# Optimization experiments

Measured on AMD Instinct MI355X. Metric: run time of the kernel, lower is better.

## Reference

```python
import jax, jax.numpy as jnp
import numpy as np

N_NODES = 200000
N_GRAPHS = 512

def gcn_conv(x, src, dst, W, b):
    # PyG GCNConv: add self-loops, symmetric normalization, linear, scatter-add
    n = x.shape[0]
    loop = jnp.arange(n)
    s = jnp.concatenate([src, loop])
    d = jnp.concatenate([dst, loop])
    deg = jax.ops.segment_sum(jnp.ones_like(d, dtype=x.dtype), d, num_segments=n)
    dinv = jnp.where(deg > 0, jax.lax.rsqrt(deg), 0.0)
    norm = dinv[s] * dinv[d]                      # [E+n]
    h = x @ W                                     # [n, out]
    msg = h[s] * norm[:, None]                    # gather on source nodes
    return jax.ops.segment_sum(msg, d, num_segments=n) + b

def setup_inputs() -> dict:
    key = jax.random.key(0)
    ks = jax.random.split(key, 24)
    def g(i, shape, scale=0.05):
        return jax.random.normal(ks[i], shape, dtype=jnp.float32) * scale
    inp = {}
    inp['x'] = jax.random.normal(ks[0], (N_NODES, 78), dtype=jnp.float32)
    inp['edge_index'] = jax.random.randint(ks[1], (2, 800000), 0, N_NODES)
    inp['batch'] = jnp.sort(jax.random.randint(ks[2], (N_NODES,), 0, N_GRAPHS))
    inp['target'] = jax.random.randint(ks[3], (N_GRAPHS, 1000), 0, 26)
    inp['W1'] = g(4, (78, 78)); inp['b1'] = jnp.zeros((78,), jnp.float32)
    inp['W2'] = g(5, (78, 156)); inp['b2'] = jnp.zeros((156,), jnp.float32)
    inp['W3'] = g(6, (156, 312)); inp['b3'] = jnp.zeros((312,), jnp.float32)
    inp['Wg1'] = g(7, (312, 1024)); inp['bg1'] = jnp.zeros((1024,), jnp.float32)
    inp['Wg2'] = g(8, (1024, 128)); inp['bg2'] = jnp.zeros((128,), jnp.float32)
    inp['emb'] = g(9, (26, 128), 1.0)
    inp['convw'] = g(10, (32, 1000, 8))  # OIW
    inp['convb'] = jnp.zeros((32,), jnp.float32)
    inp['Wxt'] = g(11, (32 * 121, 128)); inp['bxt'] = jnp.zeros((128,), jnp.float32)
    inp['Wf1'] = g(12, (256, 1024)); inp['bf1'] = jnp.zeros((1024,), jnp.float32)
    inp['Wf2'] = g(13, (1024, 512)); inp['bf2'] = jnp.zeros((512,), jnp.float32)
    inp['Wo'] = g(14, (512, 1)); inp['bo'] = jnp.zeros((1,), jnp.float32)
    return inp

def reference(x, edge_index, batch, target, W1, b1, W2, b2, W3, b3,
              Wg1, bg1, Wg2, bg2, emb, convw, convb, Wxt, bxt,
              Wf1, bf1, Wf2, bf2, Wo, bo):
    src, dst = edge_index[0], edge_index[1]
    h = jax.nn.relu(gcn_conv(x, src, dst, W1, b1))
    h = jax.nn.relu(gcn_conv(h, src, dst, W2, b2))
    h = jax.nn.relu(gcn_conv(h, src, dst, W3, b3))          # [N, 312]
    g = jax.ops.segment_max(h, batch, num_segments=N_GRAPHS)  # [B, 312]
    g = jnp.where(jnp.isfinite(g), g, 0.0)                   # guard empty segments
    g = jax.nn.relu(g @ Wg1 + bg1)                            # dropout = identity (eval)
    g = g @ Wg2 + bg2                                         # [B, 128]

    e = emb[target]                                           # [B, 1000, 128]
    c = jax.lax.conv_general_dilated(e, convw, (1,), 'VALID',
                                     dimension_numbers=('NCW', 'OIW', 'NCW'))
    c = c + convb[None, :, None]                              # [B, 32, 121]
    xt = c.reshape(-1, 32 * 121) @ Wxt + bxt                  # [B, 128]

    xc = jnp.concatenate([g, xt], axis=1)                     # [B, 256]
    xc = jax.nn.relu(xc @ Wf1 + bf1)
    xc = jax.nn.relu(xc @ Wf2 + bf2)
    return xc @ Wo + bo                                       # [B, 1]
```

## Files before the change

kernel.cpp:

```cpp
#include <hip/hip_runtime.h>
#include <hip/hip_bf16.h>

#define N_NODES 200000
#define N_EDGES 800000
#define N_GRAPHS 512

typedef __attribute__((ext_vector_type(8))) short short8v;
typedef __attribute__((ext_vector_type(4))) float f32x4;
typedef __attribute__((ext_vector_type(2))) float f32x2;
typedef __attribute__((ext_vector_type(2))) unsigned int u32x2;
typedef __attribute__((ext_vector_type(4))) unsigned int u32x4;
typedef __attribute__((ext_vector_type(4))) int i32x4;

__device__ inline float bf2f(unsigned int u) {
    union { unsigned int i; float f; } c;
    c.i = u << 16;
    return c.f;
}
__device__ inline unsigned short f2bf(float f) {
    union { __hip_bfloat16 h; unsigned short u; } c;
    c.h = __float2bfloat16(f);
    return c.u;
}


__global__ __launch_bounds__(256) void count_edges(const int* __restrict__ dst, int E,
                                                   int* __restrict__ cnt) {
    int e = blockIdx.x * 256 + threadIdx.x;
    if (e < E) atomicAdd(&cnt[dst[e]], 1);
}

__global__ __launch_bounds__(512) void block_reduce(const int* __restrict__ in, int n,
                                                    int* __restrict__ bsum) {
    __shared__ int s[512];
    int i = blockIdx.x * 512 + threadIdx.x;
    s[threadIdx.x] = (i < n) ? in[i] : 0;
    __syncthreads();
    for (int off = 256; off; off >>= 1) {
        if (threadIdx.x < off) s[threadIdx.x] += s[threadIdx.x + off];
        __syncthreads();
    }
    if (threadIdx.x == 0) bsum[blockIdx.x] = s[0];
}

__global__ __launch_bounds__(512) void scan_and_bounds(int* bsum, int nb,
                                                       const int* __restrict__ batch, int n,
                                                       int ng, int* __restrict__ gstart) {
    if (blockIdx.x == 1) {
        int b = threadIdx.x;
        if (b == 0) gstart[ng] = n;
        if (b < ng) {
            int lo = 0, hi = n;
            while (lo < hi) {
                int mid = (lo + hi) >> 1;
                if (batch[mid] < b) lo = mid + 1; else hi = mid;
            }
            gstart[b] = lo;
        }
        return;
    }
    __shared__ int buf[2][512];
    int t = threadIdx.x;
    int v = (t < nb) ? bsum[t] : 0;
    buf[0][t] = v;
    __syncthreads();
    int src = 0;
    for (int off = 1; off < 512; off <<= 1) {
        int x = buf[src][t];
        if (t >= off) x += buf[src][t - off];
        buf[src ^ 1][t] = x;
        src ^= 1;
        __syncthreads();
    }
    if (t < nb) bsum[t] = buf[src][t] - v;
}

__global__ __launch_bounds__(512) void block_scan_write(const int* __restrict__ cnt,
                                                        const int* __restrict__ bsum, int n,
                                                        int* __restrict__ rowptr,
                                                        float* __restrict__ dinv) {
    __shared__ int buf[2][512];
    int t = threadIdx.x;
    int i = blockIdx.x * 512 + t;
    int v = (i < n) ? cnt[i] : 0;
    buf[0][t] = v;
    __syncthreads();
    int src = 0;
    for (int off = 1; off < 512; off <<= 1) {
        int x = buf[src][t];
        if (t >= off) x += buf[src][t - off];
        buf[src ^ 1][t] = x;
        src ^= 1;
        __syncthreads();
    }
    int incl = buf[src][t];
    int base = bsum[blockIdx.x];
    if (i < n) {
        rowptr[i] = base + incl - v;
        dinv[i] = rsqrtf((float)(v + 1));
    }
    if (i == n - 1) rowptr[n] = base + incl;
}

__global__ __launch_bounds__(256) void fill_csr(const int* __restrict__ src,
                                                const int* __restrict__ dst, int E,
                                                const int* __restrict__ rowptr,
                                                int* __restrict__ cur, int* __restrict__ col) {
    int e = blockIdx.x * 256 + threadIdx.x;
    if (e < E) {
        int d = dst[e];
        int p = atomicAdd(&cur[d], 1);
        col[rowptr[d] + p] = src[e];
    }
}


__global__ __launch_bounds__(256) void scale_x(const float* __restrict__ x,
                                               const float* __restrict__ dinv,
                                               unsigned short* __restrict__ XS) {
    int idx = blockIdx.x * 256 + threadIdx.x;
    int v = idx / 40, c = idx % 40;
    if (v >= N_NODES) return;
    if (c == 39) {
        *(unsigned int*)(XS + (size_t)v * 80 + 78) = 0u;
        return;
    }
    float dv = dinv[v];
    f32x2 xv = *(const f32x2*)(x + (size_t)v * 78 + c * 2);
    unsigned int pack = ((unsigned int)f2bf(xv.y * dv) << 16) | f2bf(xv.x * dv);
    *(unsigned int*)(XS + (size_t)v * 80 + c * 2) = pack;
}


template <int LD, int NCH, int NPB>
__global__ __launch_bounds__(256) void agg_sum(const unsigned short* __restrict__ X,
                                               const float* __restrict__ dinv,
                                               const int* __restrict__ rowptr,
                                               const int* __restrict__ col,
                                               unsigned short* __restrict__ out) {
    int tid = threadIdx.x;
    if (tid >= NPB * NCH) return;
    int v = blockIdx.x * NPB + tid / NCH;
    int c = tid % NCH;
    if (v >= N_NODES) return;
    const unsigned short* Xc = X + c * 8;
    u32x4 xv = *(const u32x4*)(Xc + (size_t)v * LD);
    float a0 = bf2f(xv.x & 0xffffu), a1 = bf2f(xv.x >> 16);
    float a2 = bf2f(xv.y & 0xffffu), a3 = bf2f(xv.y >> 16);
    float a4 = bf2f(xv.z & 0xffffu), a5 = bf2f(xv.z >> 16);
    float a6 = bf2f(xv.w & 0xffffu), a7 = bf2f(xv.w >> 16);
    float b0 = 0.f, b1 = 0.f, b2 = 0.f, b3 = 0.f, b4 = 0.f, b5 = 0.f, b6 = 0.f, b7 = 0.f;
    int r0 = rowptr[v], r1 = rowptr[v + 1];
    int e = r0;
    for (; e + 1 < r1; e += 2) {
        int u0 = col[e], u1 = col[e + 1];
        u32x4 p = *(const u32x4*)(Xc + (size_t)u0 * LD);
        u32x4 q = *(const u32x4*)(Xc + (size_t)u1 * LD);
        a0 += bf2f(p.x & 0xffffu);
        a1 += bf2f(p.x >> 16);
        a2 += bf2f(p.y & 0xffffu);
        a3 += bf2f(p.y >> 16);
        a4 += bf2f(p.z & 0xffffu);
        a5 += bf2f(p.z >> 16);
        a6 += bf2f(p.w & 0xffffu);
        a7 += bf2f(p.w >> 16);
        b0 += bf2f(q.x & 0xffffu);
        b1 += bf2f(q.x >> 16);
        b2 += bf2f(q.y & 0xffffu);
        b3 += bf2f(q.y >> 16);
        b4 += bf2f(q.z & 0xffffu);
        b5 += bf2f(q.z >> 16);
        b6 += bf2f(q.w & 0xffffu);
        b7 += bf2f(q.w >> 16);
    }
    if (e < r1) {
        int u = col[e];
        u32x4 p = *(const u32x4*)(Xc + (size_t)u * LD);
        a0 += bf2f(p.x & 0xffffu);
        a1 += bf2f(p.x >> 16);
        a2 += bf2f(p.y & 0xffffu);
        a3 += bf2f(p.y >> 16);
        a4 += bf2f(p.z & 0xffffu);
        a5 += bf2f(p.z >> 16);
        a6 += bf2f(p.w & 0xffffu);
        a7 += bf2f(p.w >> 16);
    }
    float dv = dinv[v];
    u32x4 o;
    o.x = ((unsigned int)f2bf((a1 + b1) * dv) << 16) | f2bf((a0 + b0) * dv);
    o.y = ((unsigned int)f2bf((a3 + b3) * dv) << 16) | f2bf((a2 + b2) * dv);
    o.z = ((unsigned int)f2bf((a5 + b5) * dv) << 16) | f2bf((a4 + b4) * dv);
    o.w = ((unsigned int)f2bf((a7 + b7) * dv) << 16) | f2bf((a6 + b6) * dv);
    *(u32x4*)(out + (size_t)v * LD + c * 8) = o;
}


__device__ inline void prep_wf_body(const float* __restrict__ W, unsigned short* __restrict__ Wf,
                                    int idx, int KREAL, int NREAL, int KS, int NF) {
    if (idx >= NF * KS * 64) return;
    int lane = idx & 63, ks = (idx >> 6) % KS, nf = idx / (64 * KS);
    int k0 = ks * 32 + 8 * (lane >> 4);
    int cc = nf * 16 + (lane & 15);
    short8v t;
#pragma unroll
    for (int j = 0; j < 8; j++) {
        int k = k0 + j;
        float w = (k < KREAL && cc < NREAL) ? W[(size_t)k * NREAL + cc] : 0.f;
        t[j] = (short)f2bf(w);
    }
    *(short8v*)&Wf[(size_t)idx * 8] = t;
}

__global__ __launch_bounds__(256) void setup_misc(
    float* __restrict__ gg, const float* __restrict__ bg1, float* __restrict__ xc,
    const float* __restrict__ bg2, const float* __restrict__ bxt, float* __restrict__ f1,
    const float* __restrict__ bf1, float* __restrict__ f2, const float* __restrict__ bf2,
    const float* __restrict__ convw, unsigned short* __restrict__ CWf,
    const float* __restrict__ emb, unsigned short* __restrict__ Ef,
    const float* __restrict__ W1, unsigned short* __restrict__ W1f,
    const float* __restrict__ W2, unsigned short* __restrict__ W2f,
    const float* __restrict__ W3, unsigned short* __restrict__ W3f) {
    int b = blockIdx.x;
    int tid = threadIdx.x;
    if (b < 5632) {
        int idx = b * 256 + tid;
        int row = idx / 2816, c = idx % 2816;
        if (row >= N_GRAPHS) return;
        if (c < 1024) gg[(size_t)row * 1024 + c] = bg1[c];
        else if (c < 1280) {
            int j = c - 1024;
            xc[(size_t)row * 256 + j] = (j < 128) ? bg2[j] : bxt[j - 128];
        } else if (c < 2304)
            f1[(size_t)row * 1024 + (c - 1280)] = bf1[c - 1280];
        else
            f2[(size_t)row * 512 + (c - 2304)] = bf2[c - 2304];
        return;
    }
    b -= 5632;
    if (b < 128) {
        int idx = b * 256 + tid;
        int ks = idx >> 10, nf = (idx >> 6) & 15, lane = idx & 63;
        int k0 = ks * 32 + 8 * (lane >> 4);
        int c = nf * 16 + (lane & 15);
        int o = c >> 3, kk = c & 7;
        short8v t;
#pragma unroll
        for (int j = 0; j < 8; j++) {
            int k = k0 + j;
            float v = (k < 1000) ? convw[(size_t)o * 8000 + k * 8 + kk] : 0.f;
            t[j] = (short)f2bf(v);
        }
        *(short8v*)&CWf[(size_t)idx * 8] = t;
        return;
    }
    b -= 128;
    if (b < 14) {
        int idx = b * 256 + tid;
        if (idx >= 7 * 8 * 64) return;
        int ks = idx >> 9, nf = (idx >> 6) & 7, lane = idx & 63;
        int j0 = ks * 32 + 8 * (lane >> 4);
        int w = nf * 16 + (lane & 15);
        short8v t;
#pragma unroll
        for (int j8 = 0; j8 < 8; j8++) {
            int j = j0 + j8;
            float v = (j < 208 && w < 121) ? emb[(size_t)(j >> 3) * 128 + w + (j & 7)] : 0.f;
            t[j8] = (short)f2bf(v);
        }
        *(short8v*)&Ef[(size_t)idx * 8] = t;
        return;
    }
    b -= 14;
    if (b < 4) { prep_wf_body(W1, W1f, b * 256 + tid, 78, 78, 3, 5); return; }
    b -= 4;
    if (b < 8) { prep_wf_body(W2, W2f, b * 256 + tid, 78, 156, 3, 10); return; }
    b -= 8;
    prep_wf_body(W3, W3f, b * 256 + tid, 156, 312, 5, 20);
}


template <int NREAL, int LDA, int LDC, int NF, int KS>
__global__ __launch_bounds__(256) void gemm_mfma_node(const unsigned short* __restrict__ A,
                                                      const unsigned short* __restrict__ Wf,
                                                      const float* __restrict__ bias,
                                                      const float* __restrict__ dinv,
                                                      unsigned short* __restrict__ Cout, int M) {
    __shared__ unsigned short Bs[NF * KS * 64 * 8];
    int tid = threadIdx.x;
    for (int idx = tid; idx < NF * KS * 64; idx += 256)
        *(short8v*)&Bs[idx * 8] = *(const short8v*)&Wf[(size_t)idx * 8];
    __syncthreads();

    int lane = tid & 63, wid = tid >> 6;
    int m0 = blockIdx.x * 128 + wid * 32;
    float biasr[NF];
#pragma unroll
    for (int nf = 0; nf < NF; nf++) {
        int cc = nf * 16 + (lane & 15);
        biasr[nf] = (cc < NREAL) ? bias[cc] : 0.f;
    }
    f32x4 acc[2][NF];
#pragma unroll
    for (int mf = 0; mf < 2; mf++)
#pragma unroll
        for (int nf = 0; nf < NF; nf++) acc[mf][nf] = (f32x4){0.f, 0.f, 0.f, 0.f};

    int ra = min(m0 + (lane & 15), M - 1);
    int rb = min(m0 + 16 + (lane & 15), M - 1);
#pragma unroll
    for (int ks = 0; ks < KS; ks++) {
        int koff = ks * 32 + 8 * (lane >> 4);
        short8v a0 = *(const short8v*)(A + (size_t)ra * LDA + koff);
        short8v a1 = *(const short8v*)(A + (size_t)rb * LDA + koff);
#pragma unroll
        for (int nf = 0; nf < NF; nf++) {
            short8v b = *(const short8v*)&Bs[((nf * KS + ks) * 64 + lane) * 8];
            acc[0][nf] = __builtin_amdgcn_mfma_f32_16x16x32_bf16(a0, b, acc[0][nf], 0, 0, 0);
            acc[1][nf] = __builtin_amdgcn_mfma_f32_16x16x32_bf16(a1, b, acc[1][nf], 0, 0, 0);
        }
    }
    float dr[2][4];
#pragma unroll
    for (int mf = 0; mf < 2; mf++)
#pragma unroll
        for (int r = 0; r < 4; r++) {
            int row = m0 + mf * 16 + 4 * (lane >> 4) + r;
            dr[mf][r] = dinv[min(row, M - 1)];
        }
#pragma unroll
    for (int mf = 0; mf < 2; mf++) {
#pragma unroll
        for (int nf = 0; nf < NF; nf++) {
            int cc = nf * 16 + (lane & 15);
#pragma unroll
            for (int r = 0; r < 4; r++) {
                int row = m0 + mf * 16 + 4 * (lane >> 4) + r;
                float v = fmaxf(acc[mf][nf][r] + biasr[nf], 0.f) * dr[mf][r];
                unsigned short o = (cc < NREAL) ? f2bf(v) : (unsigned short)0;
                if (row < M) Cout[(size_t)row * LDC + cc] = o;
            }
        }
    }
}


__global__ __launch_bounds__(256) void seg_gemm_max(const unsigned short* __restrict__ A,
                                                    const unsigned short* __restrict__ Wf3,
                                                    const float* __restrict__ b3,
                                                    const int* __restrict__ gstart,
                                                    float* __restrict__ g3) {
    __shared__ unsigned short Bs[4 * 5 * 64 * 8];
    __shared__ float wmax[4][64];
    int g = blockIdx.x & 511;
    int bx = blockIdx.x >> 9;
    int c0 = bx * 64;
    int r0 = gstart[g], r1 = gstart[g + 1];
    int tid = threadIdx.x, lane = tid & 63, wid = tid >> 6;

    const unsigned short* src = Wf3 + (size_t)bx * 4 * 5 * 64 * 8;
    for (int idx = tid; idx < 1280; idx += 256)
        *(short8v*)&Bs[idx * 8] = *(const short8v*)&src[(size_t)idx * 8];
    __syncthreads();

    float biasr[4], cmax[4];
#pragma unroll
    for (int nf = 0; nf < 4; nf++) {
        int cc = c0 + nf * 16 + (lane & 15);
        biasr[nf] = (cc < 312) ? b3[cc] : 0.f;
        cmax[nf] = 0.f;
    }

    for (int mt = r0 + wid * 32; mt < r1; mt += 128) {
        f32x4 acc[2][4];
#pragma unroll
        for (int mf = 0; mf < 2; mf++)
#pragma unroll
            for (int nf = 0; nf < 4; nf++) acc[mf][nf] = (f32x4){0.f, 0.f, 0.f, 0.f};
        int ra = min(mt + (lane & 15), N_NODES - 1);
        int rb = min(mt + 16 + (lane & 15), N_NODES - 1);
#pragma unroll
        for (int ks = 0; ks < 5; ks++) {
            int koff = ks * 32 + 8 * (lane >> 4);
            short8v a0 = *(const short8v*)(A + (size_t)ra * 160 + koff);
            short8v a1 = *(const short8v*)(A + (size_t)rb * 160 + koff);
#pragma unroll
            for (int nf = 0; nf < 4; nf++) {
                short8v b = *(const short8v*)&Bs[((nf * 5 + ks) * 64 + lane) * 8];
                acc[0][nf] = __builtin_amdgcn_mfma_f32_16x16x32_bf16(a0, b, acc[0][nf], 0, 0, 0);
                acc[1][nf] = __builtin_amdgcn_mfma_f32_16x16x32_bf16(a1, b, acc[1][nf], 0, 0, 0);
            }
        }
#pragma unroll
        for (int mf = 0; mf < 2; mf++) {
#pragma unroll
            for (int nf = 0; nf < 4; nf++) {
#pragma unroll
                for (int r = 0; r < 4; r++) {
                    int row = mt + mf * 16 + 4 * (lane >> 4) + r;
                    float v = fmaxf(acc[mf][nf][r] + biasr[nf], 0.f);
                    if (row < r1) cmax[nf] = fmaxf(cmax[nf], v);
                }
            }
        }
    }
#pragma unroll
    for (int nf = 0; nf < 4; nf++) {
        float m = cmax[nf];
        m = fmaxf(m, __shfl_xor(m, 16));
        m = fmaxf(m, __shfl_xor(m, 32));
        if (lane < 16) wmax[wid][nf * 16 + lane] = m;
    }
    __syncthreads();
    if (tid < 64) {
        float m = fmaxf(fmaxf(wmax[0][tid], wmax[1][tid]), fmaxf(wmax[2][tid], wmax[3][tid]));
        int cc = c0 + tid;
        if (cc < 312) g3[(size_t)g * 312 + cc] = m;
    }
}


template <int RELUA>
__global__ __launch_bounds__(256) void gemm_splitk(const float* __restrict__ A,
                                                   const float* __restrict__ B,
                                                   float* __restrict__ C, int M, int N, int K,
                                                   int ldc, int Kc) {
    __shared__ float As[16][17];
    __shared__ float Bs[16][64];
    int bx = blockIdx.x, by = blockIdx.y, bz = blockIdx.z;
    int tid = threadIdx.x;
    int lane = tid & 63, wy = tid >> 6;
    int n0 = bx * 64, m0 = by * 16;
    int k0 = bz * Kc, k1 = min(K, k0 + Kc);
    float acc[4] = {0.f, 0.f, 0.f, 0.f};
    for (int kt = k0; kt < k1; kt += 16) {
        {
            int r = tid >> 4, kk = tid & 15;
            int gm = m0 + r, gk = kt + kk;
            float v = (gk < k1 && gm < M) ? A[(size_t)gm * K + gk] : 0.f;
            if (RELUA) v = fmaxf(v, 0.f);
            As[kk][r] = v;
        }
#pragma unroll
        for (int l = 0; l < 4; l++) {
            int kk = wy + l * 4;
            int gk = kt + kk, gn = n0 + lane;
            Bs[kk][lane] = (gk < k1 && gn < N) ? B[(size_t)gk * N + gn] : 0.f;
        }
        __syncthreads();
#pragma unroll
        for (int kk = 0; kk < 16; kk++) {
            float b = Bs[kk][lane];
#pragma unroll
            for (int r = 0; r < 4; r++) acc[r] += As[kk][wy * 4 + r] * b;
        }
        __syncthreads();
    }
    int gn = n0 + lane;
    if (gn < N) {
#pragma unroll
        for (int r = 0; r < 4; r++) {
            int gm = m0 + wy * 4 + r;
            if (gm < M) atomicAdd(&C[(size_t)gm * ldc + gn], acc[r]);
        }
    }
}


__global__ __launch_bounds__(256) void conv_mfma(const int* __restrict__ target,
                                                 const unsigned short* __restrict__ CWf,
                                                 const unsigned short* __restrict__ Ef,
                                                 const float* __restrict__ convb,
                                                 float* __restrict__ c) {
    __shared__ int tg[1024];
    __shared__ unsigned short A_lds[32 * 256];
    int n = blockIdx.x;
    int tid = threadIdx.x, lane = tid & 63, wid = tid >> 6;
    int hi = lane >> 4, l15 = lane & 15;
    for (int i = tid; i < 1024; i += 256) tg[i] = (i < 1000) ? target[n * 1000 + i] : -1;
    __syncthreads();

    f32x4 acc[2][4];
#pragma unroll
    for (int mf = 0; mf < 2; mf++)
#pragma unroll
        for (int nf = 0; nf < 4; nf++) acc[mf][nf] = (f32x4){0.f, 0.f, 0.f, 0.f};
    int r0 = l15, r1 = l15 + 16;
    for (int ks = 0; ks < 32; ks++) {
        int kk = ks * 32 + 8 * hi;
        i32x4 ta = *(const i32x4*)&tg[kk];
        i32x4 tb = *(const i32x4*)&tg[kk + 4];
        short8v a0, a1;
        a0[0] = (ta.x == r0) ? (short)0x3F80 : (short)0;
        a0[1] = (ta.y == r0) ? (short)0x3F80 : (short)0;
        a0[2] = (ta.z == r0) ? (short)0x3F80 : (short)0;
        a0[3] = (ta.w == r0) ? (short)0x3F80 : (short)0;
        a0[4] = (tb.x == r0) ? (short)0x3F80 : (short)0;
        a0[5] = (tb.y == r0) ? (short)0x3F80 : (short)0;
        a0[6] = (tb.z == r0) ? (short)0x3F80 : (short)0;
        a0[7] = (tb.w == r0) ? (short)0x3F80 : (short)0;
        a1[0] = (ta.x == r1) ? (short)0x3F80 : (short)0;
        a1[1] = (ta.y == r1) ? (short)0x3F80 : (short)0;
        a1[2] = (ta.z == r1) ? (short)0x3F80 : (short)0;
        a1[3] = (ta.w == r1) ? (short)0x3F80 : (short)0;
        a1[4] = (tb.x == r1) ? (short)0x3F80 : (short)0;
        a1[5] = (tb.y == r1) ? (short)0x3F80 : (short)0;
        a1[6] = (tb.z == r1) ? (short)0x3F80 : (short)0;
        a1[7] = (tb.w == r1) ? (short)0x3F80 : (short)0;
#pragma unroll
        for (int nf = 0; nf < 4; nf++) {
            short8v b = *(const short8v*)&CWf[((size_t)(ks * 16 + wid * 4 + nf) * 64 + lane) * 8];
            acc[0][nf] = __builtin_amdgcn_mfma_f32_16x16x32_bf16(a0, b, acc[0][nf], 0, 0, 0);
            acc[1][nf] = __builtin_amdgcn_mfma_f32_16x16x32_bf16(a1, b, acc[1][nf], 0, 0, 0);
        }
    }
#pragma unroll
    for (int mf = 0; mf < 2; mf++)
#pragma unroll
        for (int nf = 0; nf < 4; nf++) {
            int col = (wid * 4 + nf) * 16 + l15;
#pragma unroll
            for (int r = 0; r < 4; r++) {
                int row = 16 * mf + 4 * hi + r;
                A_lds[row * 256 + col] = f2bf(acc[mf][nf][r]);
            }
        }
    __syncthreads();

    f32x4 acc2[2][2];
#pragma unroll
    for (int mf = 0; mf < 2; mf++)
#pragma unroll
        for (int nf = 0; nf < 2; nf++) acc2[mf][nf] = (f32x4){0.f, 0.f, 0.f, 0.f};
#pragma unroll
    for (int ks = 0; ks < 7; ks++) {
        int j0 = ks * 32 + 8 * hi;
        int t = j0 >> 3;
        short8v a0 = *(const short8v*)&A_lds[t * 256 + l15 * 8];
        short8v a1 = *(const short8v*)&A_lds[t * 256 + (l15 + 16) * 8];
#pragma unroll
        for (int nf = 0; nf < 2; nf++) {
            short8v b = *(const short8v*)&Ef[((size_t)(ks * 8 + wid * 2 + nf) * 64 + lane) * 8];
            acc2[0][nf] = __builtin_amdgcn_mfma_f32_16x16x32_bf16(a0, b, acc2[0][nf], 0, 0, 0);
            acc2[1][nf] = __builtin_amdgcn_mfma_f32_16x16x32_bf16(a1, b, acc2[1][nf], 0, 0, 0);
        }
    }
#pragma unroll
    for (int mf = 0; mf < 2; mf++)
#pragma unroll
        for (int nf = 0; nf < 2; nf++) {
            int w = (wid * 2 + nf) * 16 + l15;
            if (w < 121) {
#pragma unroll
                for (int r = 0; r < 4; r++) {
                    int o = 16 * mf + 4 * hi + r;
                    c[(size_t)n * 3872 + o * 121 + w] = acc2[mf][nf][r] + convb[o];
                }
            }
        }
}


__global__ __launch_bounds__(256) void rowdot(const float* __restrict__ f2,
                                              const float* __restrict__ Wo,
                                              const float* __restrict__ bo,
                                              float* __restrict__ out, int M, int K) {
    int row = blockIdx.x * 4 + (threadIdx.x >> 6);
    int lane = threadIdx.x & 63;
    if (row >= M) return;
    float acc = 0.f;
    for (int k = lane; k < K; k += 64) acc += fmaxf(f2[(size_t)row * K + k], 0.f) * Wo[k];
    for (int off = 32; off; off >>= 1) acc += __shfl_down(acc, off);
    if (lane == 0) out[row] = acc + bo[0];
}


extern "C" void kernel_launch(void* const* d_in, const int* in_sizes, int n_in, void* d_out,
                              int out_size, void* d_ws, size_t ws_size, hipStream_t stream) {
    const float* x = (const float*)d_in[0];
    const int* ei = (const int*)d_in[1];
    const int* batch = (const int*)d_in[2];
    const int* target = (const int*)d_in[3];
    const float* W1 = (const float*)d_in[4];
    const float* b1 = (const float*)d_in[5];
    const float* W2 = (const float*)d_in[6];
    const float* b2 = (const float*)d_in[7];
    const float* W3 = (const float*)d_in[8];
    const float* b3 = (const float*)d_in[9];
    const float* Wg1 = (const float*)d_in[10];
    const float* bg1 = (const float*)d_in[11];
    const float* Wg2 = (const float*)d_in[12];
    const float* bg2 = (const float*)d_in[13];
    const float* emb = (const float*)d_in[14];
    const float* convw = (const float*)d_in[15];
    const float* convb = (const float*)d_in[16];
    const float* Wxt = (const float*)d_in[17];
    const float* bxt = (const float*)d_in[18];
    const float* Wf1 = (const float*)d_in[19];
    const float* bf1 = (const float*)d_in[20];
    const float* Wf2 = (const float*)d_in[21];
    const float* bf2 = (const float*)d_in[22];
    const float* Wo = (const float*)d_in[23];
    const float* bo = (const float*)d_in[24];
    float* out = (float*)d_out;

    const int N = N_NODES, E = N_EDGES;
    const int NB = (N + 511) / 512;

    char* ws = (char*)d_ws;
    size_t off = 0;
    auto alloc = [&](size_t bytes) -> char* {
        char* p = ws + off;
        off = (off + bytes + 255) & ~(size_t)255;
        return p;
    };
    int* cnt = (int*)alloc((size_t)N * 2 * 4);
    int* cur = cnt + N;
    int* rowptr = (int*)alloc((size_t)(N + 1) * 4);
    int* bsum = (int*)alloc(512 * 4);
    int* col = (int*)alloc((size_t)E * 4);
    float* dinv = (float*)alloc((size_t)N * 4);
    int* gstart = (int*)alloc((N_GRAPHS + 1) * 4);
    float* g3 = (float*)alloc((size_t)N_GRAPHS * 312 * 4);
    float* gg = (float*)alloc((size_t)N_GRAPHS * 1024 * 4);
    float* cbuf = (float*)alloc((size_t)N_GRAPHS * 3872 * 4);
    float* xc = (float*)alloc((size_t)N_GRAPHS * 256 * 4);
    float* f1 = (float*)alloc((size_t)N_GRAPHS * 1024 * 4);
    float* f2 = (float*)alloc((size_t)N_GRAPHS * 512 * 4);
    unsigned short* CWf = (unsigned short*)alloc((size_t)32768 * 8 * 2);
    unsigned short* Ef = (unsigned short*)alloc((size_t)3584 * 8 * 2);
    unsigned short* W1f = (unsigned short*)alloc((size_t)5 * 3 * 64 * 8 * 2);
    unsigned short* W2f = (unsigned short*)alloc((size_t)10 * 3 * 64 * 8 * 2);
    unsigned short* W3f = (unsigned short*)alloc((size_t)20 * 5 * 64 * 8 * 2);
    unsigned short* U = (unsigned short*)alloc((size_t)N * 160 * 2 + 512);
    unsigned short* P160 = (unsigned short*)alloc((size_t)N * 160 * 2 + 512);
    unsigned short* H1 = U + (size_t)N * 80;

    const int* srcp = ei;
    const int* dstp = ei + E;

    hipMemsetAsync(cnt, 0, (size_t)N * 2 * 4, stream);
    count_edges<<<(E + 255) / 256, 256, 0, stream>>>(dstp, E, cnt);
    block_reduce<<<NB, 512, 0, stream>>>(cnt, N, bsum);
    scan_and_bounds<<<2, 512, 0, stream>>>(bsum, NB, batch, N, N_GRAPHS, gstart);
    block_scan_write<<<NB, 512, 0, stream>>>(cnt, bsum, N, rowptr, dinv);
    fill_csr<<<(E + 255) / 256, 256, 0, stream>>>(srcp, dstp, E, rowptr, cur, col);

    setup_misc<<<5632 + 128 + 14 + 4 + 8 + 25, 256, 0, stream>>>(
        gg, bg1, xc, bg2, bxt, f1, bf1, f2, bf2, convw, CWf, emb, Ef, W1, W1f, W2, W2f, W3, W3f);

    const int MB = (N + 127) / 128;

    scale_x<<<(N * 40 + 255) / 256, 256, 0, stream>>>(x, dinv, P160);
    agg_sum<80, 10, 25><<<(N + 24) / 25, 256, 0, stream>>>(P160, dinv, rowptr, col, U);
    gemm_mfma_node<78, 80, 80, 5, 3><<<MB, 256, 0, stream>>>(U, W1f, b1, dinv, H1, N);
    agg_sum<80, 10, 25><<<(N + 24) / 25, 256, 0, stream>>>(H1, dinv, rowptr, col, P160);
    gemm_mfma_node<156, 80, 160, 10, 3><<<MB, 256, 0, stream>>>(P160, W2f, b2, dinv, U, N);
    agg_sum<160, 20, 12><<<(N + 11) / 12, 256, 0, stream>>>(U, dinv, rowptr, col, P160);
    seg_gemm_max<<<5 * N_GRAPHS, 256, 0, stream>>>(P160, W3f, b3, gstart, g3);

    gemm_splitk<0><<<dim3(16, 32, 2), 256, 0, stream>>>(g3, Wg1, gg, 512, 1024, 312, 1024, 160);
    gemm_splitk<1><<<dim3(2, 32, 8), 256, 0, stream>>>(gg, Wg2, xc, 512, 128, 1024, 256, 128);

    conv_mfma<<<N_GRAPHS, 256, 0, stream>>>(target, CWf, Ef, convb, cbuf);
    gemm_splitk<0><<<dim3(2, 32, 16), 256, 0, stream>>>(cbuf, Wxt, xc + 128, 512, 128, 3872, 256, 256);

    gemm_splitk<0><<<dim3(16, 32, 2), 256, 0, stream>>>(xc, Wf1, f1, 512, 1024, 256, 1024, 128);
    gemm_splitk<1><<<dim3(8, 32, 8), 256, 0, stream>>>(f1, Wf2, f2, 512, 512, 1024, 512, 128);
    rowdot<<<(N_GRAPHS + 3) / 4, 256, 0, stream>>>(f2, Wo, bo, out, N_GRAPHS, 512);
}
```

Before: 664.1 us.

## Replace FP32 split-K head GEMMs with bf16 MFMA kernels and fold scale_x into setup

The scalar FP32 split-K GEMMs with atomicAdd in the MLP head become bf16 MFMA kernels. Their weights are pre-swizzled in setup_misc, and bias and ReLU are fused into the epilogue, so the bias-initialisation pass goes away. The Wxt GEMM uses an explicit 11-way partial-sum buffer plus a reduce kernel. scale_x moves into the setup kernel to save a launch, and agg_sum is unrolled to 4 neighbours with independent accumulators for more memory-level parallelism. Converting the head activations to bf16 lowers precision.

```diff
diff --git a/kernel.cpp b/kernel.cpp
--- a/kernel.cpp
+++ b/kernel.cpp
@@ -8,7 +8,6 @@
 typedef __attribute__((ext_vector_type(8))) short short8v;
 typedef __attribute__((ext_vector_type(4))) float f32x4;
 typedef __attribute__((ext_vector_type(2))) float f32x2;
-typedef __attribute__((ext_vector_type(2))) unsigned int u32x2;
 typedef __attribute__((ext_vector_type(4))) unsigned int u32x4;
 typedef __attribute__((ext_vector_type(4))) int i32x4;
 
@@ -112,23 +111,6 @@
         int p = atomicAdd(&cur[d], 1);
         col[rowptr[d] + p] = src[e];
     }
-}
-
-
-__global__ __launch_bounds__(256) void scale_x(const float* __restrict__ x,
-                                               const float* __restrict__ dinv,
-                                               unsigned short* __restrict__ XS) {
-    int idx = blockIdx.x * 256 + threadIdx.x;
-    int v = idx / 40, c = idx % 40;
-    if (v >= N_NODES) return;
-    if (c == 39) {
-        *(unsigned int*)(XS + (size_t)v * 80 + 78) = 0u;
-        return;
-    }
-    float dv = dinv[v];
-    f32x2 xv = *(const f32x2*)(x + (size_t)v * 78 + c * 2);
-    unsigned int pack = ((unsigned int)f2bf(xv.y * dv) << 16) | f2bf(xv.x * dv);
-    *(unsigned int*)(XS + (size_t)v * 80 + c * 2) = pack;
 }
 
 
@@ -150,47 +132,47 @@
     float a4 = bf2f(xv.z & 0xffffu), a5 = bf2f(xv.z >> 16);
     float a6 = bf2f(xv.w & 0xffffu), a7 = bf2f(xv.w >> 16);
     float b0 = 0.f, b1 = 0.f, b2 = 0.f, b3 = 0.f, b4 = 0.f, b5 = 0.f, b6 = 0.f, b7 = 0.f;
+    float c0 = 0.f, c1 = 0.f, c2 = 0.f, c3 = 0.f, c4 = 0.f, c5 = 0.f, c6 = 0.f, c7 = 0.f;
+    float d0 = 0.f, d1 = 0.f, d2 = 0.f, d3 = 0.f, d4 = 0.f, d5 = 0.f, d6 = 0.f, d7 = 0.f;
     int r0 = rowptr[v], r1 = rowptr[v + 1];
     int e = r0;
-    for (; e + 1 < r1; e += 2) {
-        int u0 = col[e], u1 = col[e + 1];
+    for (; e + 3 < r1; e += 4) {
+        int u0 = col[e], u1 = col[e + 1], u2 = col[e + 2], u3 = col[e + 3];
         u32x4 p = *(const u32x4*)(Xc + (size_t)u0 * LD);
         u32x4 q = *(const u32x4*)(Xc + (size_t)u1 * LD);
-        a0 += bf2f(p.x & 0xffffu);
-        a1 += bf2f(p.x >> 16);
-        a2 += bf2f(p.y & 0xffffu);
-        a3 += bf2f(p.y >> 16);
-        a4 += bf2f(p.z & 0xffffu);
-        a5 += bf2f(p.z >> 16);
-        a6 += bf2f(p.w & 0xffffu);
-        a7 += bf2f(p.w >> 16);
-        b0 += bf2f(q.x & 0xffffu);
-        b1 += bf2f(q.x >> 16);
-        b2 += bf2f(q.y & 0xffffu);
-        b3 += bf2f(q.y >> 16);
-        b4 += bf2f(q.z & 0xffffu);
-        b5 += bf2f(q.z >> 16);
-        b6 += bf2f(q.w & 0xffffu);
-        b7 += bf2f(q.w >> 16);
-    }
-    if (e < r1) {
+        u32x4 s = *(const u32x4*)(Xc + (size_t)u2 * LD);
+        u32x4 t = *(const u32x4*)(Xc + (size_t)u3 * LD);
+        a0 += bf2f(p.x & 0xffffu); a1 += bf2f(p.x >> 16);
+        a2 += bf2f(p.y & 0xffffu); a3 += bf2f(p.y >> 16);
+        a4 += bf2f(p.z & 0xffffu); a5 += bf2f(p.z >> 16);
+        a6 += bf2f(p.w & 0xffffu); a7 += bf2f(p.w >> 16);
+        b0 += bf2f(q.x & 0xffffu); b1 += bf2f(q.x >> 16);
+        b2 += bf2f(q.y & 0xffffu); b3 += bf2f(q.y >> 16);
+        b4 += bf2f(q.z & 0xffffu); b5 += bf2f(q.z >> 16);
+        b6 += bf2f(q.w & 0xffffu); b7 += bf2f(q.w >> 16);
+        c0 += bf2f(s.x & 0xffffu); c1 += bf2f(s.x >> 16);
+        c2 += bf2f(s.y & 0xffffu); c3 += bf2f(s.y >> 16);
+        c4 += bf2f(s.z & 0xffffu); c5 += bf2f(s.z >> 16);
+        c6 += bf2f(s.w & 0xffffu); c7 += bf2f(s.w >> 16);
+        d0 += bf2f(t.x & 0xffffu); d1 += bf2f(t.x >> 16);
+        d2 += bf2f(t.y & 0xffffu); d3 += bf2f(t.y >> 16);
+        d4 += bf2f(t.z & 0xffffu); d5 += bf2f(t.z >> 16);
+        d6 += bf2f(t.w & 0xffffu); d7 += bf2f(t.w >> 16);
+    }
+    for (; e < r1; ++e) {
         int u = col[e];
         u32x4 p = *(const u32x4*)(Xc + (size_t)u * LD);
-        a0 += bf2f(p.x & 0xffffu);
-        a1 += bf2f(p.x >> 16);
-        a2 += bf2f(p.y & 0xffffu);
-        a3 += bf2f(p.y >> 16);
-        a4 += bf2f(p.z & 0xffffu);
-        a5 += bf2f(p.z >> 16);
-        a6 += bf2f(p.w & 0xffffu);
-        a7 += bf2f(p.w >> 16);
+        a0 += bf2f(p.x & 0xffffu); a1 += bf2f(p.x >> 16);
+        a2 += bf2f(p.y & 0xffffu); a3 += bf2f(p.y >> 16);
+        a4 += bf2f(p.z & 0xffffu); a5 += bf2f(p.z >> 16);
+        a6 += bf2f(p.w & 0xffffu); a7 += bf2f(p.w >> 16);
     }
     float dv = dinv[v];
     u32x4 o;
-    o.x = ((unsigned int)f2bf((a1 + b1) * dv) << 16) | f2bf((a0 + b0) * dv);
-    o.y = ((unsigned int)f2bf((a3 + b3) * dv) << 16) | f2bf((a2 + b2) * dv);
-    o.z = ((unsigned int)f2bf((a5 + b5) * dv) << 16) | f2bf((a4 + b4) * dv);
-    o.w = ((unsigned int)f2bf((a7 + b7) * dv) << 16) | f2bf((a6 + b6) * dv);
+    o.x = ((unsigned int)f2bf((a1 + b1 + c1 + d1) * dv) << 16) | f2bf((a0 + b0 + c0 + d0) * dv);
+    o.y = ((unsigned int)f2bf((a3 + b3 + c3 + d3) * dv) << 16) | f2bf((a2 + b2 + c2 + d2) * dv);
+    o.z = ((unsigned int)f2bf((a5 + b5 + c5 + d5) * dv) << 16) | f2bf((a4 + b4 + c4 + d4) * dv);
+    o.w = ((unsigned int)f2bf((a7 + b7 + c7 + d7) * dv) << 16) | f2bf((a6 + b6 + c6 + d6) * dv);
     *(u32x4*)(out + (size_t)v * LD + c * 8) = o;
 }
 
@@ -211,32 +193,38 @@
     *(short8v*)&Wf[(size_t)idx * 8] = t;
 }
 
+#define SETUP_SCALE_BLOCKS 31250
+#define SETUP_BLOCKS (SETUP_SCALE_BLOCKS + 128 + 14 + 4 + 8 + 25 + 160 + 64 + 242 + 128 + 256)
+
 __global__ __launch_bounds__(256) void setup_misc(
-    float* __restrict__ gg, const float* __restrict__ bg1, float* __restrict__ xc,
-    const float* __restrict__ bg2, const float* __restrict__ bxt, float* __restrict__ f1,
-    const float* __restrict__ bf1, float* __restrict__ f2, const float* __restrict__ bf2,
+    const float* __restrict__ x, const float* __restrict__ dinv, unsigned short* __restrict__ XS,
     const float* __restrict__ convw, unsigned short* __restrict__ CWf,
     const float* __restrict__ emb, unsigned short* __restrict__ Ef,
     const float* __restrict__ W1, unsigned short* __restrict__ W1f,
     const float* __restrict__ W2, unsigned short* __restrict__ W2f,
-    const float* __restrict__ W3, unsigned short* __restrict__ W3f) {
+    const float* __restrict__ W3, unsigned short* __restrict__ W3f,
+    const float* __restrict__ Wg1, unsigned short* __restrict__ Wg1f,
+    const float* __restrict__ Wg2, unsigned short* __restrict__ Wg2f,
+    const float* __restrict__ Wxt, unsigned short* __restrict__ Wxtf,
+    const float* __restrict__ Wf1, unsigned short* __restrict__ Wf1f,
+    const float* __restrict__ Wf2, unsigned short* __restrict__ Wf2f) {
     int b = blockIdx.x;
     int tid = threadIdx.x;
-    if (b < 5632) {
+    if (b < SETUP_SCALE_BLOCKS) {
         int idx = b * 256 + tid;
-        int row = idx / 2816, c = idx % 2816;
-        if (row >= N_GRAPHS) return;
-        if (c < 1024) gg[(size_t)row * 1024 + c] = bg1[c];
-        else if (c < 1280) {
-            int j = c - 1024;
-            xc[(size_t)row * 256 + j] = (j < 128) ? bg2[j] : bxt[j - 128];
-        } else if (c < 2304)
-            f1[(size_t)row * 1024 + (c - 1280)] = bf1[c - 1280];
-        else
-            f2[(size_t)row * 512 + (c - 2304)] = bf2[c - 2304];
+        int v = idx / 40, c = idx % 40;
+        if (v >= N_NODES) return;
+        if (c == 39) {
+            *(unsigned int*)(XS + (size_t)v * 80 + 78) = 0u;
+            return;
+        }
+        float dv = dinv[v];
+        f32x2 xv = *(const f32x2*)(x + (size_t)v * 78 + c * 2);
+        unsigned int pack = ((unsigned int)f2bf(xv.y * dv) << 16) | f2bf(xv.x * dv);
+        *(unsigned int*)(XS + (size_t)v * 80 + c * 2) = pack;
         return;
     }
-    b -= 5632;
+    b -= SETUP_SCALE_BLOCKS;
     if (b < 128) {
         int idx = b * 256 + tid;
         int ks = idx >> 10, nf = (idx >> 6) & 15, lane = idx & 63;
@@ -275,7 +263,17 @@
     b -= 4;
     if (b < 8) { prep_wf_body(W2, W2f, b * 256 + tid, 78, 156, 3, 10); return; }
     b -= 8;
-    prep_wf_body(W3, W3f, b * 256 + tid, 156, 312, 5, 20);
+    if (b < 25) { prep_wf_body(W3, W3f, b * 256 + tid, 156, 312, 5, 20); return; }
+    b -= 25;
+    if (b < 160) { prep_wf_body(Wg1, Wg1f, b * 256 + tid, 312, 1024, 10, 64); return; }
+    b -= 160;
+    if (b < 64) { prep_wf_body(Wg2, Wg2f, b * 256 + tid, 1024, 128, 32, 8); return; }
+    b -= 64;
+    if (b < 242) { prep_wf_body(Wxt, Wxtf, b * 256 + tid, 3872, 128, 121, 8); return; }
+    b -= 242;
+    if (b < 128) { prep_wf_body(Wf1, Wf1f, b * 256 + tid, 256, 1024, 8, 64); return; }
+    b -= 128;
+    prep_wf_body(Wf2, Wf2f, b * 256 + tid, 1024, 512, 32, 32);
 }
 
 
@@ -419,50 +417,126 @@
 }
 
 
-template <int RELUA>
-__global__ __launch_bounds__(256) void gemm_splitk(const float* __restrict__ A,
-                                                   const float* __restrict__ B,
-                                                   float* __restrict__ C, int M, int N, int K,
-                                                   int ldc, int Kc) {
-    __shared__ float As[16][17];
-    __shared__ float Bs[16][64];
-    int bx = blockIdx.x, by = blockIdx.y, bz = blockIdx.z;
-    int tid = threadIdx.x;
-    int lane = tid & 63, wy = tid >> 6;
-    int n0 = bx * 64, m0 = by * 16;
-    int k0 = bz * Kc, k1 = min(K, k0 + Kc);
-    float acc[4] = {0.f, 0.f, 0.f, 0.f};
-    for (int kt = k0; kt < k1; kt += 16) {
-        {
-            int r = tid >> 4, kk = tid & 15;
-            int gm = m0 + r, gk = kt + kk;
-            float v = (gk < k1 && gm < M) ? A[(size_t)gm * K + gk] : 0.f;
-            if (RELUA) v = fmaxf(v, 0.f);
-            As[kk][r] = v;
-        }
-#pragma unroll
-        for (int l = 0; l < 4; l++) {
-            int kk = wy + l * 4;
-            int gk = kt + kk, gn = n0 + lane;
-            Bs[kk][lane] = (gk < k1 && gn < N) ? B[(size_t)gk * N + gn] : 0.f;
-        }
-        __syncthreads();
-#pragma unroll
-        for (int kk = 0; kk < 16; kk++) {
-            float b = Bs[kk][lane];
-#pragma unroll
-            for (int r = 0; r < 4; r++) acc[r] += As[kk][wy * 4 + r] * b;
-        }
-        __syncthreads();
-    }
-    int gn = n0 + lane;
-    if (gn < N) {
-#pragma unroll
-        for (int r = 0; r < 4; r++) {
-            int gm = m0 + wy * 4 + r;
-            if (gm < M) atomicAdd(&C[(size_t)gm * ldc + gn], acc[r]);
-        }
-    }
+template <int ACT, int KS, int K, int LDC, int COFF>
+__global__ __launch_bounds__(256) void head_mfma(const float* __restrict__ A,
+                                                 const unsigned short* __restrict__ Wf,
+                                                 const float* __restrict__ bias,
+                                                 float* __restrict__ C) {
+    int tid = threadIdx.x, lane = tid & 63, wid = tid >> 6;
+    int hi = lane >> 4, l15 = lane & 15;
+    int m0 = blockIdx.y * 128 + wid * 32;
+    int n0 = blockIdx.x * 64;
+    f32x4 acc[2][4];
+#pragma unroll
+    for (int mf = 0; mf < 2; mf++)
+#pragma unroll
+        for (int nf = 0; nf < 4; nf++) acc[mf][nf] = (f32x4){0.f, 0.f, 0.f, 0.f};
+    const float* Ar0 = A + (size_t)(m0 + l15) * K;
+    const float* Ar1 = A + (size_t)(m0 + 16 + l15) * K;
+#pragma unroll 2
+    for (int ks = 0; ks < KS; ks++) {
+        int k0 = ks * 32 + 8 * hi;
+        f32x4 p0 = *(const f32x4*)(Ar0 + k0);
+        f32x4 p1 = *(const f32x4*)(Ar0 + k0 + 4);
+        f32x4 q0 = *(const f32x4*)(Ar1 + k0);
+        f32x4 q1 = *(const f32x4*)(Ar1 + k0 + 4);
+        short8v a0, a1;
+        a0[0] = (short)f2bf(p0.x); a0[1] = (short)f2bf(p0.y);
+        a0[2] = (short)f2bf(p0.z); a0[3] = (short)f2bf(p0.w);
+        a0[4] = (short)f2bf(p1.x); a0[5] = (short)f2bf(p1.y);
+        a0[6] = (short)f2bf(p1.z); a0[7] = (short)f2bf(p1.w);
+        a1[0] = (short)f2bf(q0.x); a1[1] = (short)f2bf(q0.y);
+        a1[2] = (short)f2bf(q0.z); a1[3] = (short)f2bf(q0.w);
+        a1[4] = (short)f2bf(q1.x); a1[5] = (short)f2bf(q1.y);
+        a1[6] = (short)f2bf(q1.z); a1[7] = (short)f2bf(q1.w);
+#pragma unroll
+        for (int nf = 0; nf < 4; nf++) {
+            int nfg = blockIdx.x * 4 + nf;
+            short8v b = *(const short8v*)&Wf[((size_t)(nfg * KS + ks) * 64 + lane) * 8];
+            acc[0][nf] = __builtin_amdgcn_mfma_f32_16x16x32_bf16(a0, b, acc[0][nf], 0, 0, 0);
+            acc[1][nf] = __builtin_amdgcn_mfma_f32_16x16x32_bf16(a1, b, acc[1][nf], 0, 0, 0);
+        }
+    }
+#pragma unroll
+    for (int mf = 0; mf < 2; mf++) {
+#pragma unroll
+        for (int nf = 0; nf < 4; nf++) {
+            int cc = n0 + nf * 16 + l15;
+            float bj = bias[cc];
+#pragma unroll
+            for (int r = 0; r < 4; r++) {
+                int row = m0 + mf * 16 + 4 * hi + r;
+                float v = acc[mf][nf][r] + bj;
+                if (ACT) v = fmaxf(v, 0.f);
+                C[(size_t)row * LDC + COFF + cc] = v;
+            }
+        }
+    }
+}
+
+__global__ __launch_bounds__(256) void head_mfma_part(const float* __restrict__ A,
+                                                      const unsigned short* __restrict__ Wf,
+                                                      float* __restrict__ cpart) {
+    int tid = threadIdx.x, lane = tid & 63, wid = tid >> 6;
+    int hi = lane >> 4, l15 = lane & 15;
+    int m0 = blockIdx.y * 128 + wid * 32;
+    int n0 = blockIdx.x * 64;
+    int kz = blockIdx.z;
+    f32x4 acc[2][4];
+#pragma unroll
+    for (int mf = 0; mf < 2; mf++)
+#pragma unroll
+        for (int nf = 0; nf < 4; nf++) acc[mf][nf] = (f32x4){0.f, 0.f, 0.f, 0.f};
+    const float* Ar0 = A + (size_t)(m0 + l15) * 3872;
+    const float* Ar1 = A + (size_t)(m0 + 16 + l15) * 3872;
+    for (int i = 0; i < 11; i++) {
+        int ks = kz * 11 + i;
+        int k0 = ks * 32 + 8 * hi;
+        f32x4 p0 = *(const f32x4*)(Ar0 + k0);
+        f32x4 p1 = *(const f32x4*)(Ar0 + k0 + 4);
+        f32x4 q0 = *(const f32x4*)(Ar1 + k0);
+        f32x4 q1 = *(const f32x4*)(Ar1 + k0 + 4);
+        short8v a0, a1;
+        a0[0] = (short)f2bf(p0.x); a0[1] = (short)f2bf(p0.y);
+        a0[2] = (short)f2bf(p0.z); a0[3] = (short)f2bf(p0.w);
+        a0[4] = (short)f2bf(p1.x); a0[5] = (short)f2bf(p1.y);
+        a0[6] = (short)f2bf(p1.z); a0[7] = (short)f2bf(p1.w);
+        a1[0] = (short)f2bf(q0.x); a1[1] = (short)f2bf(q0.y);
+        a1[2] = (short)f2bf(q0.z); a1[3] = (short)f2bf(q0.w);
+        a1[4] = (short)f2bf(q1.x); a1[5] = (short)f2bf(q1.y);
+        a1[6] = (short)f2bf(q1.z); a1[7] = (short)f2bf(q1.w);
+#pragma unroll
+        for (int nf = 0; nf < 4; nf++) {
+            int nfg = blockIdx.x * 4 + nf;
+            short8v b = *(const short8v*)&Wf[((size_t)(nfg * 121 + ks) * 64 + lane) * 8];
+            acc[0][nf] = __builtin_amdgcn_mfma_f32_16x16x32_bf16(a0, b, acc[0][nf], 0, 0, 0);
+            acc[1][nf] = __builtin_amdgcn_mfma_f32_16x16x32_bf16(a1, b, acc[1][nf], 0, 0, 0);
+        }
+    }
+#pragma unroll
+    for (int mf = 0; mf < 2; mf++) {
+#pragma unroll
+        for (int nf = 0; nf < 4; nf++) {
+            int cc = n0 + nf * 16 + l15;
+#pragma unroll
+            for (int r = 0; r < 4; r++) {
+                int row = m0 + mf * 16 + 4 * hi + r;
+                cpart[((size_t)kz * 512 + row) * 128 + cc] = acc[mf][nf][r];
+            }
+        }
+    }
+}
+
+__global__ __launch_bounds__(256) void reduce_xt(const float* __restrict__ cpart,
+                                                 const float* __restrict__ bxt,
+                                                 float* __restrict__ xc) {
+    int idx = blockIdx.x * 256 + threadIdx.x;
+    if (idx >= 512 * 128) return;
+    int row = idx >> 7, c = idx & 127;
+    float s = bxt[c];
+#pragma unroll
+    for (int k = 0; k < 11; k++) s += cpart[((size_t)k * 512 + row) * 128 + c];
+    xc[(size_t)row * 256 + 128 + c] = s;
 }
 
 
@@ -568,7 +642,7 @@
     int lane = threadIdx.x & 63;
     if (row >= M) return;
     float acc = 0.f;
-    for (int k = lane; k < K; k += 64) acc += fmaxf(f2[(size_t)row * K + k], 0.f) * Wo[k];
+    for (int k = lane; k < K; k += 64) acc += f2[(size_t)row * K + k] * Wo[k];
     for (int off = 32; off; off >>= 1) acc += __shfl_down(acc, off);
     if (lane == 0) out[row] = acc + bo[0];
 }
@@ -626,11 +700,17 @@
     float* xc = (float*)alloc((size_t)N_GRAPHS * 256 * 4);
     float* f1 = (float*)alloc((size_t)N_GRAPHS * 1024 * 4);
     float* f2 = (float*)alloc((size_t)N_GRAPHS * 512 * 4);
+    float* cpart = (float*)alloc((size_t)11 * 512 * 128 * 4);
     unsigned short* CWf = (unsigned short*)alloc((size_t)32768 * 8 * 2);
     unsigned short* Ef = (unsigned short*)alloc((size_t)3584 * 8 * 2);
     unsigned short* W1f = (unsigned short*)alloc((size_t)5 * 3 * 64 * 8 * 2);
     unsigned short* W2f = (unsigned short*)alloc((size_t)10 * 3 * 64 * 8 * 2);
     unsigned short* W3f = (unsigned short*)alloc((size_t)20 * 5 * 64 * 8 * 2);
+    unsigned short* Wg1f = (unsigned short*)alloc((size_t)64 * 10 * 64 * 8 * 2);
+    unsigned short* Wg2f = (unsigned short*)alloc((size_t)8 * 32 * 64 * 8 * 2);
+    unsigned short* Wxtf = (unsigned short*)alloc((size_t)8 * 121 * 64 * 8 * 2);
+    unsigned short* Wf1f = (unsigned short*)alloc((size_t)64 * 8 * 64 * 8 * 2);
+    unsigned short* Wf2f = (unsigned short*)alloc((size_t)32 * 32 * 64 * 8 * 2);
     unsigned short* U = (unsigned short*)alloc((size_t)N * 160 * 2 + 512);
     unsigned short* P160 = (unsigned short*)alloc((size_t)N * 160 * 2 + 512);
     unsigned short* H1 = U + (size_t)N * 80;
@@ -645,12 +725,12 @@
     block_scan_write<<<NB, 512, 0, stream>>>(cnt, bsum, N, rowptr, dinv);
     fill_csr<<<(E + 255) / 256, 256, 0, stream>>>(srcp, dstp, E, rowptr, cur, col);
 
-    setup_misc<<<5632 + 128 + 14 + 4 + 8 + 25, 256, 0, stream>>>(
-        gg, bg1, xc, bg2, bxt, f1, bf1, f2, bf2, convw, CWf, emb, Ef, W1, W1f, W2, W2f, W3, W3f);
+    setup_misc<<<SETUP_BLOCKS, 256, 0, stream>>>(x, dinv, P160, convw, CWf, emb, Ef, W1, W1f, W2,
+                                                 W2f, W3, W3f, Wg1, Wg1f, Wg2, Wg2f, Wxt, Wxtf,
+                                                 Wf1, Wf1f, Wf2, Wf2f);
 
     const int MB = (N + 127) / 128;
 
-    scale_x<<<(N * 40 + 255) / 256, 256, 0, stream>>>(x, dinv, P160);
     agg_sum<80, 10, 25><<<(N + 24) / 25, 256, 0, stream>>>(P160, dinv, rowptr, col, U);
     gemm_mfma_node<78, 80, 80, 5, 3><<<MB, 256, 0, stream>>>(U, W1f, b1, dinv, H1, N);
     agg_sum<80, 10, 25><<<(N + 24) / 25, 256, 0, stream>>>(H1, dinv, rowptr, col, P160);
@@ -658,13 +738,14 @@
     agg_sum<160, 20, 12><<<(N + 11) / 12, 256, 0, stream>>>(U, dinv, rowptr, col, P160);
     seg_gemm_max<<<5 * N_GRAPHS, 256, 0, stream>>>(P160, W3f, b3, gstart, g3);
 
-    gemm_splitk<0><<<dim3(16, 32, 2), 256, 0, stream>>>(g3, Wg1, gg, 512, 1024, 312, 1024, 160);
-    gemm_splitk<1><<<dim3(2, 32, 8), 256, 0, stream>>>(gg, Wg2, xc, 512, 128, 1024, 256, 128);
+    head_mfma<1, 10, 312, 1024, 0><<<dim3(16, 4), 256, 0, stream>>>(g3, Wg1f, bg1, gg);
+    head_mfma<0, 32, 1024, 256, 0><<<dim3(2, 4), 256, 0, stream>>>(gg, Wg2f, bg2, xc);
 
     conv_mfma<<<N_GRAPHS, 256, 0, stream>>>(target, CWf, Ef, convb, cbuf);
-    gemm_splitk<0><<<dim3(2, 32, 16), 256, 0, stream>>>(cbuf, Wxt, xc + 128, 512, 128, 3872, 256, 256);
-
-    gemm_splitk<0><<<dim3(16, 32, 2), 256, 0, stream>>>(xc, Wf1, f1, 512, 1024, 256, 1024, 128);
-    gemm_splitk<1><<<dim3(8, 32, 8), 256, 0, stream>>>(f1, Wf2, f2, 512, 512, 1024, 512, 128);
+    head_mfma_part<<<dim3(2, 4, 11), 256, 0, stream>>>(cbuf, Wxtf, cpart);
+    reduce_xt<<<256, 256, 0, stream>>>(cpart, bxt, xc);
+
+    head_mfma<1, 8, 256, 1024, 0><<<dim3(16, 4), 256, 0, stream>>>(xc, Wf1f, bf1, f1);
+    head_mfma<1, 32, 1024, 512, 0><<<dim3(8, 4), 256, 0, stream>>>(f1, Wf2f, bf2, f2);
     rowdot<<<(N_GRAPHS + 3) / 4, 256, 0, stream>>>(f2, Wo, bo, out, N_GRAPHS, 512);
 }
```

Measured after the change: 602.5 us. 9.3% less time.
